# Performance work log

Measured on AMD Instinct MI355X. Metric: run time of the kernel, lower is better.

Reference implementation:

```python
import jax, jax.numpy as jnp
import numpy as np

B, T = 64, 512
VSZ, EMB, HID, ENC = 32000, 512, 1024, 1024  # ENC = enc_hid*2

def setup_inputs() -> dict:
    key = jax.random.key(0)
    ks = jax.random.split(key, 14)
    s = 0.02
    emb_table = jax.random.normal(ks[4], (VSZ, EMB), jnp.float32) * s
    emb_table = emb_table.at[0].set(0.0)  # padding_idx=0
    return {
        "tok": jax.random.randint(ks[0], (B,), 0, VSZ),
        "h": jax.random.normal(ks[1], (1, B, HID), jnp.float32),
        "c": jax.random.normal(ks[2], (1, B, HID), jnp.float32),
        "enc_out": jax.random.normal(ks[3], (B, T, ENC), jnp.float32),
        "emb_table": emb_table,
        "attn_W": jax.random.normal(ks[5], (HID, ENC + HID), jnp.float32) * s,
        "attn_b": jnp.zeros((HID,), jnp.float32),
        "v_W": jax.random.normal(ks[6], (1, HID), jnp.float32) * s,
        "W_ih": jax.random.normal(ks[7], (4 * HID, EMB + ENC), jnp.float32) * s,
        "W_hh": jax.random.normal(ks[8], (4 * HID, HID), jnp.float32) * s,
        "b_ih": jnp.zeros((4 * HID,), jnp.float32),
        "b_hh": jnp.zeros((4 * HID,), jnp.float32),
        "fc_W": jax.random.normal(ks[9], (VSZ, HID + ENC + EMB), jnp.float32) * s,
        "fc_b": jnp.zeros((VSZ,), jnp.float32),
    }

def reference(tok, h, c, enc_out, emb_table, attn_W, attn_b, v_W,
              W_ih, W_hh, b_ih, b_hh, fc_W, fc_b):
    # embedding lookup (dropout = identity, eval mode)
    e = emb_table[tok]                       # [B, EMB]
    h0, c0 = h[0], c[0]                      # [B, HID]
    b, t, _ = enc_out.shape

    # --- Bahdanau additive attention ---
    h_rep = jnp.broadcast_to(h0[:, None, :], (b, t, h0.shape[-1]))
    cat = jnp.concatenate([h_rep, enc_out], axis=2)          # [B, T, HID+ENC]
    energy = jnp.tanh(jnp.einsum('btf,hf->bth', cat, attn_W) + attn_b)
    scores = jnp.einsum('bth,h->bt', energy, v_W[0])         # [B, T]
    weights = jax.nn.softmax(scores, axis=1)
    ctx = jnp.einsum('bt,bte->be', weights, enc_out)          # [B, ENC]

    # --- single-step LSTM (PyTorch gate order i, f, g, o) ---
    x = jnp.concatenate([e, ctx], axis=1)                     # [B, EMB+ENC]
    gates = x @ W_ih.T + b_ih + h0 @ W_hh.T + b_hh            # [B, 4*HID]
    i, f, g, o = jnp.split(gates, 4, axis=1)
    i, f, o = jax.nn.sigmoid(i), jax.nn.sigmoid(f), jax.nn.sigmoid(o)
    g = jnp.tanh(g)
    c_new = f * c0 + i * g
    h_new = o * jnp.tanh(c_new)

    # --- concat + output projection ---
    pred = jnp.concatenate([h_new, ctx, e], axis=1) @ fc_W.T + fc_b  # [B, VSZ]
    return pred, h_new[None], c_new[None]
```

## Files before the change

### kernel.cpp

```cpp
#include <hip/hip_runtime.h>
#include <hip/hip_bf16.h>
#include <cstddef>

typedef __attribute__((ext_vector_type(4))) float f32x4;
typedef __attribute__((ext_vector_type(8))) short s16x8;

#define B_    64
#define T_    512
#define EMB_  512
#define HID_  1024
#define ENC_  1024
#define VSZ_  32000
#define PRED_N (B_ * VSZ_)

__device__ __forceinline__ unsigned short f2bf(float f) {
  __hip_bfloat16 h = __float2bfloat16(f);
  return __builtin_bit_cast(unsigned short, h);
}

__device__ __forceinline__ s16x8 pack8(f32x4 lo, f32x4 hi) {
  s16x8 r;
  r[0] = (short)f2bf(lo[0]); r[1] = (short)f2bf(lo[1]);
  r[2] = (short)f2bf(lo[2]); r[3] = (short)f2bf(lo[3]);
  r[4] = (short)f2bf(hi[0]); r[5] = (short)f2bf(hi[1]);
  r[6] = (short)f2bf(hi[2]); r[7] = (short)f2bf(hi[3]);
  return r;
}

__global__ void k1a_emb(const int* __restrict__ tok, const float* __restrict__ emb,
                        float* __restrict__ x2, unsigned short* __restrict__ xcat) {
  int b = blockIdx.x;
  int t = tok[b];
  for (int c = threadIdx.x; c < EMB_; c += blockDim.x) {
    float e = emb[(size_t)t * EMB_ + c];
    x2[b * 1536 + c] = e;
    xcat[b * 2560 + 2048 + c] = f2bf(e);
  }
}

__global__ void k1_rowdot(const float* __restrict__ W, int ldw,
                          const float* __restrict__ bias, const float* __restrict__ bias2,
                          const float* __restrict__ h0, float* __restrict__ out, int N) {
  __shared__ float hs[HID_];
  int b = blockIdx.y;
  for (int i = threadIdx.x; i < HID_; i += 256) hs[i] = h0[b * HID_ + i];
  __syncthreads();
  int g = threadIdx.x >> 4, ln = threadIdx.x & 15;
  int r = blockIdx.x * 16 + g;
  const float* wr = W + (size_t)r * ldw;
  float acc = 0.f;
  for (int k = ln * 4; k < HID_; k += 64) {
    f32x4 w4 = *(const f32x4*)(wr + k);
    f32x4 h4 = *(const f32x4*)(hs + k);
    acc += w4[0] * h4[0] + w4[1] * h4[1] + w4[2] * h4[2] + w4[3] * h4[3];
  }
  acc += __shfl_xor(acc, 1);
  acc += __shfl_xor(acc, 2);
  acc += __shfl_xor(acc, 4);
  acc += __shfl_xor(acc, 8);
  if (ln == 0) {
    float bs = bias[r] + (bias2 ? bias2[r] : 0.f);
    out[(size_t)b * N + r] = acc + bs;
  }
}

__global__ __launch_bounds__(256, 2) void k2_scores(
    const float* __restrict__ enc, const float* __restrict__ attnW,
    const float* __restrict__ hW, const float* __restrict__ vW,
    float* __restrict__ scores) {
  __shared__ unsigned short As[128][32];
  __shared__ unsigned short Bs[128][32];
  const int tid = threadIdx.x;
  const int rb = blockIdx.x;
  const int cb = blockIdx.y;
  const int wave = tid >> 6, lane = tid & 63;
  const int wr = (wave >> 1) * 64, wc = (wave & 1) * 64;
  const int l16 = lane & 15, l4 = lane >> 4;
  const int row0 = rb * 128, h0 = cb * 128;
  const int srow = tid >> 1, soff = (tid & 1) * 16;

  const float* ag = enc + (size_t)(row0 + srow) * ENC_ + soff;
  const float* bg = attnW + (size_t)(h0 + srow) * 2048 + HID_ + soff;

  f32x4 acc[4][4] = {};

  for (int kt = 0; kt < ENC_ / 32; ++kt) {
    f32x4 a0 = *(const f32x4*)(ag + 0);
    f32x4 a1 = *(const f32x4*)(ag + 4);
    f32x4 a2 = *(const f32x4*)(ag + 8);
    f32x4 a3 = *(const f32x4*)(ag + 12);
    f32x4 b0 = *(const f32x4*)(bg + 0);
    f32x4 b1 = *(const f32x4*)(bg + 4);
    f32x4 b2 = *(const f32x4*)(bg + 8);
    f32x4 b3 = *(const f32x4*)(bg + 12);
    ag += 32; bg += 32;
    s16x8 av0 = pack8(a0, a1), av1 = pack8(a2, a3);
    s16x8 bv0 = pack8(b0, b1), bv1 = pack8(b2, b3);
    __syncthreads();
    *(s16x8*)&As[srow][soff]     = av0;
    *(s16x8*)&As[srow][soff + 8] = av1;
    *(s16x8*)&Bs[srow][soff]     = bv0;
    *(s16x8*)&Bs[srow][soff + 8] = bv1;
    __syncthreads();
    s16x8 af[4], bf[4];
#pragma unroll
    for (int m = 0; m < 4; ++m) af[m] = *(const s16x8*)&As[wr + m * 16 + l16][l4 * 8];
#pragma unroll
    for (int n = 0; n < 4; ++n) bf[n] = *(const s16x8*)&Bs[wc + n * 16 + l16][l4 * 8];
#pragma unroll
    for (int m = 0; m < 4; ++m)
#pragma unroll
      for (int n = 0; n < 4; ++n)
        acc[m][n] = __builtin_amdgcn_mfma_f32_16x16x32_bf16(af[m], bf[n], acc[m][n], 0, 0, 0);
  }

  const float* hWb = hW + (size_t)(rb >> 2) * HID_;
  float vv[4], hb[4];
#pragma unroll
  for (int n = 0; n < 4; ++n) {
    int hcol = h0 + wc + n * 16 + l16;
    vv[n] = vW[hcol];
    hb[n] = hWb[hcol];
  }
#pragma unroll
  for (int m = 0; m < 4; ++m) {
#pragma unroll
    for (int j = 0; j < 4; ++j) {
      float p = 0.f;
#pragma unroll
      for (int n = 0; n < 4; ++n)
        p += vv[n] * tanhf(acc[m][n][j] + hb[n]);
      p += __shfl_xor(p, 1);
      p += __shfl_xor(p, 2);
      p += __shfl_xor(p, 4);
      p += __shfl_xor(p, 8);
      if (l16 == 0)
        atomicAdd(&scores[row0 + wr + m * 16 + l4 * 4 + j], p);
    }
  }
}

__global__ void k3a_softmax(const float* __restrict__ scores, float* __restrict__ weights) {
  int b = blockIdx.x, lane = threadIdx.x;
  float s[8];
  float mx = -3.4e38f;
#pragma unroll
  for (int i = 0; i < 8; ++i) { s[i] = scores[b * T_ + lane + i * 64]; mx = fmaxf(mx, s[i]); }
#pragma unroll
  for (int off = 1; off < 64; off <<= 1) mx = fmaxf(mx, __shfl_xor(mx, off));
  float sum = 0.f;
#pragma unroll
  for (int i = 0; i < 8; ++i) { s[i] = expf(s[i] - mx); sum += s[i]; }
#pragma unroll
  for (int off = 1; off < 64; off <<= 1) sum += __shfl_xor(sum, off);
  float inv = 1.f / sum;
#pragma unroll
  for (int i = 0; i < 8; ++i) weights[b * T_ + lane + i * 64] = s[i] * inv;
}

__global__ void k3b_ctx(const float* __restrict__ weights, const float* __restrict__ enc,
                        float* __restrict__ x2, unsigned short* __restrict__ xcat) {
  __shared__ float w[T_];
  int b = blockIdx.x >> 2;
  int col = (blockIdx.x & 3) * 256 + threadIdx.x;
  for (int i = threadIdx.x; i < T_; i += 256) w[i] = weights[b * T_ + i];
  __syncthreads();
  const float* e = enc + (size_t)b * T_ * ENC_ + col;
  float a0 = 0, a1 = 0, a2 = 0, a3 = 0;
  for (int t = 0; t < T_; t += 4) {
    a0 += w[t]     * e[(size_t)t * ENC_];
    a1 += w[t + 1] * e[(size_t)(t + 1) * ENC_];
    a2 += w[t + 2] * e[(size_t)(t + 2) * ENC_];
    a3 += w[t + 3] * e[(size_t)(t + 3) * ENC_];
  }
  float acc = (a0 + a1) + (a2 + a3);
  x2[b * 1536 + 512 + col] = acc;
  xcat[b * 2560 + 1024 + col] = f2bf(acc);
}

__global__ __launch_bounds__(256) void k4_gates(
    const float* __restrict__ x2, const float* __restrict__ Wih,
    const float* __restrict__ hWhh, float* __restrict__ gates) {
  __shared__ float Ws[64][36];
  __shared__ float Xs[64][36];
  const int tid = threadIdx.x;
  const int jb = blockIdx.x;
  const int j0 = (tid & 15) * 4, b0 = (tid >> 4) * 4;
  const int row = tid >> 2, c0 = (tid & 3) * 8;
  const float* wg = Wih + (size_t)(jb * 64 + row) * 1536 + c0;
  const float* xg = x2 + (size_t)row * 1536 + c0;
  float acc[4][4] = {{0.f}};
  for (int kt = 0; kt < 48; ++kt) {
    f32x4 w0 = *(const f32x4*)(wg);
    f32x4 w1 = *(const f32x4*)(wg + 4);
    f32x4 x0 = *(const f32x4*)(xg);
    f32x4 x1 = *(const f32x4*)(xg + 4);
    wg += 32; xg += 32;
    __syncthreads();
    *(f32x4*)&Ws[row][c0]     = w0;
    *(f32x4*)&Ws[row][c0 + 4] = w1;
    *(f32x4*)&Xs[row][c0]     = x0;
    *(f32x4*)&Xs[row][c0 + 4] = x1;
    __syncthreads();
#pragma unroll
    for (int k4 = 0; k4 < 8; ++k4) {
      f32x4 wv[4], xv[4];
#pragma unroll
      for (int i = 0; i < 4; ++i) wv[i] = *(const f32x4*)&Ws[j0 + i][k4 * 4];
#pragma unroll
      for (int l = 0; l < 4; ++l) xv[l] = *(const f32x4*)&Xs[b0 + l][k4 * 4];
#pragma unroll
      for (int i = 0; i < 4; ++i)
#pragma unroll
        for (int l = 0; l < 4; ++l)
          acc[i][l] += wv[i][0] * xv[l][0] + wv[i][1] * xv[l][1] +
                       wv[i][2] * xv[l][2] + wv[i][3] * xv[l][3];
    }
  }
#pragma unroll
  for (int i = 0; i < 4; ++i)
#pragma unroll
    for (int l = 0; l < 4; ++l) {
      int j = jb * 64 + j0 + i, bb = b0 + l;
      gates[(size_t)bb * 4096 + j] = acc[i][l] + hWhh[(size_t)bb * 4096 + j];
    }
}

__global__ void k4b_lstm(const float* __restrict__ gates, const float* __restrict__ cin,
                         float* __restrict__ out, unsigned short* __restrict__ xcat) {
  int b = blockIdx.x;
  for (int j = threadIdx.x; j < HID_; j += blockDim.x) {
    float ig = gates[(size_t)b * 4096 + j];
    float fg = gates[(size_t)b * 4096 + 1024 + j];
    float gg = gates[(size_t)b * 4096 + 2048 + j];
    float og = gates[(size_t)b * 4096 + 3072 + j];
    float i = 1.f / (1.f + expf(-ig));
    float f = 1.f / (1.f + expf(-fg));
    float g = tanhf(gg);
    float o = 1.f / (1.f + expf(-og));
    float c0 = cin[(size_t)b * 1024 + j];
    float cn = f * c0 + i * g;
    float hn = o * tanhf(cn);
    out[PRED_N + (size_t)b * 1024 + j] = hn;
    out[PRED_N + 65536 + (size_t)b * 1024 + j] = cn;
    xcat[b * 2560 + j] = f2bf(hn);
  }
}

__global__ __launch_bounds__(256, 2) void k5_pred(
    const unsigned short* __restrict__ xcat, const float* __restrict__ fcW,
    const float* __restrict__ fcb, float* __restrict__ pred) {
  __shared__ unsigned short As[64][32];
  __shared__ unsigned short Bs[128][32];
  const int tid = threadIdx.x;
  const int cb = blockIdx.x;
  const int wave = tid >> 6, lane = tid & 63;
  const int wr = (wave >> 1) * 32, wc = (wave & 1) * 64;
  const int l16 = lane & 15, l4 = lane >> 4;
  const int v0 = cb * 128;
  const int arow = tid >> 2, aoff = (tid & 3) * 8;
  const int brow = tid >> 1, boff = (tid & 1) * 16;

  const unsigned short* ag = xcat + (size_t)arow * 2560 + aoff;
  const float* bg = fcW + (size_t)(v0 + brow) * 2560 + boff;

  f32x4 acc[2][4] = {};

  for (int kt = 0; kt < 2560 / 32; ++kt) {
    s16x8 av = *(const s16x8*)(ag);
    ag += 32;
    f32x4 b0 = *(const f32x4*)(bg + 0);
    f32x4 b1 = *(const f32x4*)(bg + 4);
    f32x4 b2 = *(const f32x4*)(bg + 8);
    f32x4 b3 = *(const f32x4*)(bg + 12);
    bg += 32;
    s16x8 bv0 = pack8(b0, b1), bv1 = pack8(b2, b3);
    __syncthreads();
    *(s16x8*)&As[arow][aoff]     = av;
    *(s16x8*)&Bs[brow][boff]     = bv0;
    *(s16x8*)&Bs[brow][boff + 8] = bv1;
    __syncthreads();
    s16x8 af[2], bf[4];
#pragma unroll
    for (int m = 0; m < 2; ++m) af[m] = *(const s16x8*)&As[wr + m * 16 + l16][l4 * 8];
#pragma unroll
    for (int n = 0; n < 4; ++n) bf[n] = *(const s16x8*)&Bs[wc + n * 16 + l16][l4 * 8];
#pragma unroll
    for (int m = 0; m < 2; ++m)
#pragma unroll
      for (int n = 0; n < 4; ++n)
        acc[m][n] = __builtin_amdgcn_mfma_f32_16x16x32_bf16(af[m], bf[n], acc[m][n], 0, 0, 0);
  }
#pragma unroll
  for (int n = 0; n < 4; ++n) {
    int v = v0 + wc + n * 16 + l16;
    float fb = fcb[v];
#pragma unroll
    for (int m = 0; m < 2; ++m) {
      int br = wr + m * 16 + l4 * 4;
#pragma unroll
      for (int j = 0; j < 4; ++j)
        pred[(size_t)(br + j) * VSZ_ + v] = acc[m][n][j] + fb;
    }
  }
}

extern "C" void kernel_launch(void* const* d_in, const int* in_sizes, int n_in,
                              void* d_out, int out_size, void* d_ws, size_t ws_size,
                              hipStream_t stream) {
  (void)in_sizes; (void)n_in; (void)out_size; (void)ws_size;
  const int*   tok   = (const int*)  d_in[0];
  const float* h     = (const float*)d_in[1];
  const float* c     = (const float*)d_in[2];
  const float* enc   = (const float*)d_in[3];
  const float* emb   = (const float*)d_in[4];
  const float* attnW = (const float*)d_in[5];
  const float* attnb = (const float*)d_in[6];
  const float* vW    = (const float*)d_in[7];
  const float* Wih   = (const float*)d_in[8];
  const float* Whh   = (const float*)d_in[9];
  const float* bih   = (const float*)d_in[10];
  const float* bhh   = (const float*)d_in[11];
  const float* fcW   = (const float*)d_in[12];
  const float* fcb   = (const float*)d_in[13];
  float* out = (float*)d_out;

  float* scores  = (float*)d_ws;
  float* weights = scores + 32768;
  float* hW      = weights + 32768;
  float* hWhh    = hW + 64 * 1024;
  float* x2      = hWhh + 64 * 4096;
  float* gates   = x2 + 64 * 1536;
  unsigned short* xcat = (unsigned short*)(gates + 64 * 4096);

  hipMemsetAsync(scores, 0, 32768 * sizeof(float), stream);
  k1a_emb<<<64, 128, 0, stream>>>(tok, emb, x2, xcat);
  k1_rowdot<<<dim3(64, 64), 256, 0, stream>>>(attnW, 2048, attnb, nullptr, h, hW, 1024);
  k1_rowdot<<<dim3(256, 64), 256, 0, stream>>>(Whh, 1024, bih, bhh, h, hWhh, 4096);
  k2_scores<<<dim3(256, 8), 256, 0, stream>>>(enc, attnW, hW, vW, scores);
  k3a_softmax<<<64, 64, 0, stream>>>(scores, weights);
  k3b_ctx<<<256, 256, 0, stream>>>(weights, enc, x2, xcat);
  k4_gates<<<64, 256, 0, stream>>>(x2, Wih, hWhh, gates);
  k4b_lstm<<<64, 256, 0, stream>>>(gates, c, out, xcat);
  k5_pred<<<250, 256, 0, stream>>>(xcat, fcW, fcb, out);
}
```

Before: 1.052 ms.

## Double-buffer attention GEMM with swizzled LDS, LDS-free pred GEMM, unroll ctx

```diff
diff --git a/kernel.cpp b/kernel.cpp
--- a/kernel.cpp
+++ b/kernel.cpp
@@ -25,6 +25,10 @@
   r[4] = (short)f2bf(hi[0]); r[5] = (short)f2bf(hi[1]);
   r[6] = (short)f2bf(hi[2]); r[7] = (short)f2bf(hi[3]);
   return r;
+}
+
+__device__ __forceinline__ int swz(int row, int s) {
+  return row * 64 + ((s ^ ((row >> 1) & 3)) << 4);
 }
 
 __global__ void k1a_emb(const int* __restrict__ tok, const float* __restrict__ emb,
@@ -64,12 +68,37 @@
   }
 }
 
+#define K2_LOAD(S, kt) { const float* _pa = ag0 + (kt) * 32;                 \
+    S##a0 = *(const f32x4*)(_pa);      S##a1 = *(const f32x4*)(_pa + 4);     \
+    S##a2 = *(const f32x4*)(_pa + 8);  S##a3 = *(const f32x4*)(_pa + 12);    \
+    const float* _pb = bg0 + (kt) * 32;                                      \
+    S##b0 = *(const f32x4*)(_pb);      S##b1 = *(const f32x4*)(_pb + 4);     \
+    S##b2 = *(const f32x4*)(_pb + 8);  S##b3 = *(const f32x4*)(_pb + 12); }
+
+#define K2_PW(S, L) {                                                        \
+    s16x8 _v0 = pack8(S##a0, S##a1), _v1 = pack8(S##a2, S##a3);              \
+    s16x8 _w0 = pack8(S##b0, S##b1), _w1 = pack8(S##b2, S##b3);              \
+    *(s16x8*)((L) + waA0) = _v0; *(s16x8*)((L) + waA1) = _v1;                \
+    *(s16x8*)((L) + waB0) = _w0; *(s16x8*)((L) + waB1) = _w1; }
+
+#define K2_COMP(L) {                                                         \
+    s16x8 af[4], bf[4];                                                      \
+    _Pragma("unroll")                                                        \
+    for (int m = 0; m < 4; ++m) af[m] = *(const s16x8*)((L) + raA[m]);       \
+    _Pragma("unroll")                                                        \
+    for (int n = 0; n < 4; ++n) bf[n] = *(const s16x8*)((L) + raB[n]);       \
+    _Pragma("unroll")                                                        \
+    for (int m = 0; m < 4; ++m)                                              \
+      _Pragma("unroll")                                                      \
+      for (int n = 0; n < 4; ++n)                                            \
+        acc[m][n] = __builtin_amdgcn_mfma_f32_16x16x32_bf16(af[m], bf[n], acc[m][n], 0, 0, 0); }
+
 __global__ __launch_bounds__(256, 2) void k2_scores(
     const float* __restrict__ enc, const float* __restrict__ attnW,
     const float* __restrict__ hW, const float* __restrict__ vW,
     float* __restrict__ scores) {
-  __shared__ unsigned short As[128][32];
-  __shared__ unsigned short Bs[128][32];
+  __shared__ unsigned char lds0[16384];
+  __shared__ unsigned char lds1[16384];
   const int tid = threadIdx.x;
   const int rb = blockIdx.x;
   const int cb = blockIdx.y;
@@ -77,41 +106,38 @@
   const int wr = (wave >> 1) * 64, wc = (wave & 1) * 64;
   const int l16 = lane & 15, l4 = lane >> 4;
   const int row0 = rb * 128, h0 = cb * 128;
-  const int srow = tid >> 1, soff = (tid & 1) * 16;
-
-  const float* ag = enc + (size_t)(row0 + srow) * ENC_ + soff;
-  const float* bg = attnW + (size_t)(h0 + srow) * 2048 + HID_ + soff;
-
+  const int srow = tid >> 1;
+  const int s0 = (tid & 1) * 2;
+
+  const float* ag0 = enc   + (size_t)(row0 + srow) * ENC_  + (tid & 1) * 16;
+  const float* bg0 = attnW + (size_t)(h0  + srow) * 2048 + HID_ + (tid & 1) * 16;
+
+  const int waA0 = swz(srow, s0), waA1 = swz(srow, s0 + 1);
+  const int waB0 = 8192 + waA0,   waB1 = 8192 + waA1;
+  int raA[4], raB[4];
+#pragma unroll
+  for (int m = 0; m < 4; ++m) raA[m] = swz(wr + m * 16 + l16, l4);
+#pragma unroll
+  for (int n = 0; n < 4; ++n) raB[n] = 8192 + swz(wc + n * 16 + l16, l4);
+
+  f32x4 Xa0, Xa1, Xa2, Xa3, Xb0, Xb1, Xb2, Xb3;
+  f32x4 Ya0, Ya1, Ya2, Ya3, Yb0, Yb1, Yb2, Yb3;
   f32x4 acc[4][4] = {};
 
-  for (int kt = 0; kt < ENC_ / 32; ++kt) {
-    f32x4 a0 = *(const f32x4*)(ag + 0);
-    f32x4 a1 = *(const f32x4*)(ag + 4);
-    f32x4 a2 = *(const f32x4*)(ag + 8);
-    f32x4 a3 = *(const f32x4*)(ag + 12);
-    f32x4 b0 = *(const f32x4*)(bg + 0);
-    f32x4 b1 = *(const f32x4*)(bg + 4);
-    f32x4 b2 = *(const f32x4*)(bg + 8);
-    f32x4 b3 = *(const f32x4*)(bg + 12);
-    ag += 32; bg += 32;
-    s16x8 av0 = pack8(a0, a1), av1 = pack8(a2, a3);
-    s16x8 bv0 = pack8(b0, b1), bv1 = pack8(b2, b3);
+  K2_LOAD(X, 0);
+  K2_PW(X, lds0);
+  K2_LOAD(Y, 1);
+  __syncthreads();
+
+  for (int kt2 = 0; kt2 < 16; ++kt2) {
+    if (kt2 < 15) K2_LOAD(X, 2 * kt2 + 2);
+    K2_COMP(lds0);
+    K2_PW(Y, lds1);
     __syncthreads();
-    *(s16x8*)&As[srow][soff]     = av0;
-    *(s16x8*)&As[srow][soff + 8] = av1;
-    *(s16x8*)&Bs[srow][soff]     = bv0;
-    *(s16x8*)&Bs[srow][soff + 8] = bv1;
+    if (kt2 < 15) K2_LOAD(Y, 2 * kt2 + 3);
+    K2_COMP(lds1);
+    if (kt2 < 15) K2_PW(X, lds0);
     __syncthreads();
-    s16x8 af[4], bf[4];
-#pragma unroll
-    for (int m = 0; m < 4; ++m) af[m] = *(const s16x8*)&As[wr + m * 16 + l16][l4 * 8];
-#pragma unroll
-    for (int n = 0; n < 4; ++n) bf[n] = *(const s16x8*)&Bs[wc + n * 16 + l16][l4 * 8];
-#pragma unroll
-    for (int m = 0; m < 4; ++m)
-#pragma unroll
-      for (int n = 0; n < 4; ++n)
-        acc[m][n] = __builtin_amdgcn_mfma_f32_16x16x32_bf16(af[m], bf[n], acc[m][n], 0, 0, 0);
   }
 
   const float* hWb = hW + (size_t)(rb >> 2) * HID_;
@@ -166,14 +192,18 @@
   for (int i = threadIdx.x; i < T_; i += 256) w[i] = weights[b * T_ + i];
   __syncthreads();
   const float* e = enc + (size_t)b * T_ * ENC_ + col;
-  float a0 = 0, a1 = 0, a2 = 0, a3 = 0;
-  for (int t = 0; t < T_; t += 4) {
+  float a0 = 0, a1 = 0, a2 = 0, a3 = 0, a4 = 0, a5 = 0, a6 = 0, a7 = 0;
+  for (int t = 0; t < T_; t += 8) {
     a0 += w[t]     * e[(size_t)t * ENC_];
     a1 += w[t + 1] * e[(size_t)(t + 1) * ENC_];
     a2 += w[t + 2] * e[(size_t)(t + 2) * ENC_];
     a3 += w[t + 3] * e[(size_t)(t + 3) * ENC_];
-  }
-  float acc = (a0 + a1) + (a2 + a3);
+    a4 += w[t + 4] * e[(size_t)(t + 4) * ENC_];
+    a5 += w[t + 5] * e[(size_t)(t + 5) * ENC_];
+    a6 += w[t + 6] * e[(size_t)(t + 6) * ENC_];
+    a7 += w[t + 7] * e[(size_t)(t + 7) * ENC_];
+  }
+  float acc = ((a0 + a1) + (a2 + a3)) + ((a4 + a5) + (a6 + a7));
   x2[b * 1536 + 512 + col] = acc;
   xcat[b * 2560 + 1024 + col] = f2bf(acc);
 }
@@ -247,62 +277,50 @@
   }
 }
 
-__global__ __launch_bounds__(256, 2) void k5_pred(
+__global__ __launch_bounds__(256) void k5_pred(
     const unsigned short* __restrict__ xcat, const float* __restrict__ fcW,
     const float* __restrict__ fcb, float* __restrict__ pred) {
-  __shared__ unsigned short As[64][32];
-  __shared__ unsigned short Bs[128][32];
   const int tid = threadIdx.x;
-  const int cb = blockIdx.x;
   const int wave = tid >> 6, lane = tid & 63;
-  const int wr = (wave >> 1) * 32, wc = (wave & 1) * 64;
   const int l16 = lane & 15, l4 = lane >> 4;
-  const int v0 = cb * 128;
-  const int arow = tid >> 2, aoff = (tid & 3) * 8;
-  const int brow = tid >> 1, boff = (tid & 1) * 16;
-
-  const unsigned short* ag = xcat + (size_t)arow * 2560 + aoff;
-  const float* bg = fcW + (size_t)(v0 + brow) * 2560 + boff;
-
-  f32x4 acc[2][4] = {};
-
-  for (int kt = 0; kt < 2560 / 32; ++kt) {
-    s16x8 av = *(const s16x8*)(ag);
-    ag += 32;
-    f32x4 b0 = *(const f32x4*)(bg + 0);
-    f32x4 b1 = *(const f32x4*)(bg + 4);
-    f32x4 b2 = *(const f32x4*)(bg + 8);
-    f32x4 b3 = *(const f32x4*)(bg + 12);
-    bg += 32;
-    s16x8 bv0 = pack8(b0, b1), bv1 = pack8(b2, b3);
-    __syncthreads();
-    *(s16x8*)&As[arow][aoff]     = av;
-    *(s16x8*)&Bs[brow][boff]     = bv0;
-    *(s16x8*)&Bs[brow][boff + 8] = bv1;
-    __syncthreads();
-    s16x8 af[2], bf[4];
-#pragma unroll
-    for (int m = 0; m < 2; ++m) af[m] = *(const s16x8*)&As[wr + m * 16 + l16][l4 * 8];
-#pragma unroll
-    for (int n = 0; n < 4; ++n) bf[n] = *(const s16x8*)&Bs[wc + n * 16 + l16][l4 * 8];
-#pragma unroll
-    for (int m = 0; m < 2; ++m)
-#pragma unroll
-      for (int n = 0; n < 4; ++n)
-        acc[m][n] = __builtin_amdgcn_mfma_f32_16x16x32_bf16(af[m], bf[n], acc[m][n], 0, 0, 0);
-  }
-#pragma unroll
-  for (int n = 0; n < 4; ++n) {
-    int v = v0 + wc + n * 16 + l16;
-    float fb = fcb[v];
-#pragma unroll
-    for (int m = 0; m < 2; ++m) {
-      int br = wr + m * 16 + l4 * 4;
-#pragma unroll
-      for (int j = 0; j < 4; ++j)
-        pred[(size_t)(br + j) * VSZ_ + v] = acc[m][n][j] + fb;
+  const int vrow = blockIdx.x * 64 + wave * 16 + l16;
+  const float* bg = fcW + (size_t)vrow * 2560 + l4 * 8;
+  const unsigned short* ag = xcat + (size_t)l16 * 2560 + l4 * 8;
+
+  f32x4 acc[4] = {};
+
+  f32x4 nb0 = *(const f32x4*)(bg);
+  f32x4 nb1 = *(const f32x4*)(bg + 4);
+  s16x8 na0 = *(const s16x8*)(ag);
+  s16x8 na1 = *(const s16x8*)(ag + 16 * 2560);
+  s16x8 na2 = *(const s16x8*)(ag + 32 * 2560);
+  s16x8 na3 = *(const s16x8*)(ag + 48 * 2560);
+
+  for (int kt = 0; kt < 80; ++kt) {
+    f32x4 b0 = nb0, b1 = nb1;
+    s16x8 a0 = na0, a1 = na1, a2 = na2, a3 = na3;
+    if (kt < 79) {
+      bg += 32; ag += 32;
+      nb0 = *(const f32x4*)(bg);
+      nb1 = *(const f32x4*)(bg + 4);
+      na0 = *(const s16x8*)(ag);
+      na1 = *(const s16x8*)(ag + 16 * 2560);
+      na2 = *(const s16x8*)(ag + 32 * 2560);
+      na3 = *(const s16x8*)(ag + 48 * 2560);
     }
-  }
+    s16x8 bv = pack8(b0, b1);
+    acc[0] = __builtin_amdgcn_mfma_f32_16x16x32_bf16(a0, bv, acc[0], 0, 0, 0);
+    acc[1] = __builtin_amdgcn_mfma_f32_16x16x32_bf16(a1, bv, acc[1], 0, 0, 0);
+    acc[2] = __builtin_amdgcn_mfma_f32_16x16x32_bf16(a2, bv, acc[2], 0, 0, 0);
+    acc[3] = __builtin_amdgcn_mfma_f32_16x16x32_bf16(a3, bv, acc[3], 0, 0, 0);
+  }
+
+  float fb = fcb[vrow];
+#pragma unroll
+  for (int m = 0; m < 4; ++m)
+#pragma unroll
+    for (int j = 0; j < 4; ++j)
+      pred[(size_t)(m * 16 + l4 * 4 + j) * VSZ_ + vrow] = acc[m][j] + fb;
 }
 
 extern "C" void kernel_launch(void* const* d_in, const int* in_sizes, int n_in,
@@ -342,5 +360,5 @@
   k3b_ctx<<<256, 256, 0, stream>>>(weights, enc, x2, xcat);
   k4_gates<<<64, 256, 0, stream>>>(x2, Wih, hWhh, gates);
   k4b_lstm<<<64, 256, 0, stream>>>(gates, c, out, xcat);
-  k5_pred<<<250, 256, 0, stream>>>(xcat, fcW, fcb, out);
-}
+  k5_pred<<<500, 256, 0, stream>>>(xcat, fcW, fcb, out);
+}
```

Result: faster. 1.014 ms (-3.7%).
